# Optimization experiments

Hardware: AMD Instinct MI355X
Metric: run time of the kernel (lower is better)

## Reference

```python
import jax, jax.numpy as jnp
import numpy as np

B, C, TX, TY = 32, 384, 512, 2048
NL, K = 2, 3
EPS = 1e-5


def _ln(x, g, b):
    # channel-wise LayerNorm over dim 1 of [B, C, T]
    m = jnp.mean(x, axis=1, keepdims=True)
    v = jnp.mean((x - m) ** 2, axis=1, keepdims=True)
    return (x - m) * jax.lax.rsqrt(v + EPS) * g[None, :, None] + b[None, :, None]


def _conv(x, w, b):
    # x: [B, C, T], w: [O, I, K] -> 'SAME' padding == kernel_size // 2 for odd K
    y = jax.lax.conv_general_dilated(x, w, (1,), 'SAME',
                                     dimension_numbers=('NCH', 'OIH', 'NCH'))
    return y + b[None, :, None]


def _variance_predictor(x, mask, lng, lnb, cw, cb, ow, ob):
    # NL x (LayerNorm -> Conv1d -> SiLU -> [dropout=identity in eval]) * mask
    for i in range(NL):
        h = _conv(_ln(x, lng[i], lnb[i]), cw[i], cb[i])
        x = jax.nn.silu(h) * mask
    return _conv(x, ow, ob) * mask  # [B, 1, T]


def setup_inputs() -> dict:
    key = jax.random.key(0)
    it = iter(jax.random.split(key, 16))
    s = 0.02
    d = {}
    d['x'] = jax.random.normal(next(it), (B, C, TX), jnp.float32)
    d['x_mask'] = jnp.ones((B, 1, TX), jnp.float32)
    d['y_mask'] = jnp.ones((B, 1, TY), jnp.float32)
    d['pitch'] = jax.random.normal(next(it), (B, C, TY), jnp.float32)
    d['energy'] = jax.random.normal(next(it), (B, C, TY), jnp.float32)
    d['path'] = jax.random.uniform(next(it), (B, TX, TY), jnp.float32)
    for p in ('dur', 'pit', 'ene'):
        d[p + '_lng'] = jnp.ones((NL, C), jnp.float32)
        d[p + '_lnb'] = jnp.zeros((NL, C), jnp.float32)
        d[p + '_cw'] = jax.random.normal(next(it), (NL, C, C, K), jnp.float32) * s
        d[p + '_cb'] = jnp.zeros((NL, C), jnp.float32)
        d[p + '_ow'] = jax.random.normal(next(it), (1, C, 1), jnp.float32) * s
        d[p + '_ob'] = jnp.zeros((1,), jnp.float32)
    return d


def reference(x, x_mask, y_mask, pitch, energy, path,
              dur_lng, dur_lnb, dur_cw, dur_cb, dur_ow, dur_ob,
              pit_lng, pit_lnb, pit_cw, pit_cb, pit_ow, pit_ob,
              ene_lng, ene_lnb, ene_cw, ene_cb, ene_ow, ene_ob):
    dur_pred = _variance_predictor(x, x_mask, dur_lng, dur_lnb, dur_cw, dur_cb, dur_ow, dur_ob)
    # LengthRegulator: bmm against duration path matrix [B, TX, TY]
    xe = jnp.einsum('bct,bty->bcy', x, path)  # [B, C, TY]
    pitch_pred = _variance_predictor(xe, y_mask, pit_lng, pit_lnb, pit_cw, pit_cb, pit_ow, pit_ob)
    energy_pred = _variance_predictor(xe, y_mask, ene_lng, ene_lnb, ene_cw, ene_cb, ene_ow, ene_ob)
    out = xe + pitch + energy
    return (out, dur_pred, pitch_pred, energy_pred)
```

## Files before the change

kernel.cpp:

```cpp
#include <hip/hip_runtime.h>

#define B_ 32
#define C_ 384
#define TX_ 512
#define TY_ 2048
#define EPS_ 1e-5f
#define LAY_ ((size_t)(36 * 1536 * 8))

typedef __attribute__((ext_vector_type(8))) short short8;
typedef __attribute__((ext_vector_type(4))) float f32x4;

#define MFMA(a, b, c) __builtin_amdgcn_mfma_f32_16x16x32_bf16(a, b, c, 0, 0, 0)

#define WAITV(N) do { asm volatile("s_waitcnt vmcnt(" #N ")"); \
                      __builtin_amdgcn_sched_barrier(0); } while (0)
#define WAITLK(N) do { asm volatile("s_waitcnt lgkmcnt(" #N ")"); \
                       __builtin_amdgcn_sched_barrier(0); } while (0)
#define SB() __builtin_amdgcn_sched_barrier(0)

typedef unsigned int u32;
__device__ __forceinline__ void gl_lds16(const void* g, void* l) {
    __builtin_amdgcn_global_load_lds(
        (const __attribute__((address_space(1))) u32*)g,
        (__attribute__((address_space(3))) u32*)l, 16, 0, 0);
}

__device__ inline unsigned short f2bf(float f) {
    union { float f; unsigned int u; } v; v.f = f;
    unsigned int r = v.u + 0x7fffu + ((v.u >> 16) & 1u);
    return (unsigned short)(r >> 16);
}
__device__ inline float bf2f(unsigned short s) {
    union { float f; unsigned int u; } v; v.u = ((unsigned int)s) << 16;
    return v.f;
}

template<bool INBF>
__device__ inline float ldx(const void* p, size_t i) {
    if constexpr (INBF) return bf2f(((const unsigned short*)p)[i]);
    else return ((const float*)p)[i];
}

__global__ __launch_bounds__(256) void pack_w2(const float* cw0, const float* cw1,
                                               const float* cw2, const float* g0,
                                               const float* g1, const float* g2,
                                               unsigned short* wp) {
    int idx = blockIdx.x * 256 + threadIdx.x;
    const int NG = 6 * 36 * 384 * 4;
    if (idx >= NG) return;
    int lg = idx & 3;
    int o = (idx >> 2) % 384;
    int c = ((idx >> 2) / 384) % 36;
    int lay = (idx >> 2) / (384 * 36);
    int k = c / 12, ib = c % 12;
    int pr = lay >> 1, l = lay & 1;
    const float* cw = ((pr == 0) ? cw0 : (pr == 1) ? cw1 : cw2) + (size_t)l * C_ * C_ * 3;
    const float* g  = ((pr == 0) ? g0  : (pr == 1) ? g1  : g2)  + (size_t)l * C_;
    const int i0 = ib * 32 + lg * 8;
    short8 v;
    #pragma unroll
    for (int e = 0; e < 8; e++)
        v[e] = (short)f2bf(cw[((size_t)o * C_ + i0 + e) * 3 + k] * g[i0 + e]);
    *(short8*)&wp[(size_t)idx * 8] = v;
}

__global__ __launch_bounds__(256) void bias_fold(
    const float* cw0, const float* cw1, const float* cw2,
    const float* be0, const float* be1, const float* be2,
    const float* cb0, const float* cb1, const float* cb2,
    float* biasT, float* bc0, float* bc2) {
    int idx = blockIdx.x * 256 + threadIdx.x;
    if (idx >= 6 * 384) return;
    int o = idx % 384, lay = idx / 384;
    int pr = lay >> 1, l = lay & 1;
    const float* cw = ((pr == 0) ? cw0 : (pr == 1) ? cw1 : cw2)
                      + (size_t)l * C_ * C_ * 3 + (size_t)o * C_ * 3;
    const float* be = ((pr == 0) ? be0 : (pr == 1) ? be1 : be2) + (size_t)l * C_;
    const float* cb = ((pr == 0) ? cb0 : (pr == 1) ? cb1 : cb2) + (size_t)l * C_;
    float s0 = 0.f, s1 = 0.f, s2 = 0.f;
    for (int i = 0; i < C_; i++) {
        const float b = be[i];
        s0 += cw[i * 3 + 0] * b; s1 += cw[i * 3 + 1] * b; s2 += cw[i * 3 + 2] * b;
    }
    biasT[idx] = cb[o] + s0 + s1 + s2;
    bc0[idx] = s0; bc2[idx] = s2;
}

__global__ __launch_bounds__(256) void pack_x2(const float* x, unsigned short* xp) {
    int idx = blockIdx.x * 256 + threadIdx.x;
    const int NG = B_ * 16 * 384 * 4;
    if (idx >= NG) return;
    int lg = idx & 3;
    int c = (idx >> 2) % 384;
    int q = ((idx >> 2) / 384) % 16;
    int b = (idx >> 2) / (384 * 16);
    const float* src = x + ((size_t)b * C_ + c) * TX_ + q * 32 + lg * 8;
    short8 v;
    #pragma unroll
    for (int e = 0; e < 8; e++) v[e] = (short)f2bf(src[e]);
    *(short8*)&xp[(size_t)idx * 8] = v;
}

__global__ __launch_bounds__(256) void ln_stats_f32(const float* x, float2* st, int T) {
    __shared__ float r1[4][64], r2[4][64];
    int b = blockIdx.y, t0 = blockIdx.x * 64;
    int tl = threadIdx.x & 63, g = threadIdx.x >> 6;
    int t = t0 + tl;
    const float* p = x + (size_t)b * C_ * T + t;
    float s = 0.f, ss = 0.f;
    for (int c = g; c < C_; c += 4) { float v = p[(size_t)c * T]; s += v; ss += v * v; }
    r1[g][tl] = s; r2[g][tl] = ss;
    __syncthreads();
    if (threadIdx.x < 64) {
        float s1 = r1[0][tl] + r1[1][tl] + r1[2][tl] + r1[3][tl];
        float s2 = r2[0][tl] + r2[1][tl] + r2[2][tl] + r2[3][tl];
        float m = s1 * (1.f / C_);
        float var = s2 * (1.f / C_) - m * m;
        st[(size_t)b * T + t0 + tl] = make_float2(m, rsqrtf(var + EPS_));
    }
}

template<bool INBF>
__global__ __launch_bounds__(512, 2) void fused_vp(
    const void* __restrict__ Xin, const float2* __restrict__ stin,
    const unsigned short* __restrict__ W2lay,
    const float* __restrict__ bT,
    const float* __restrict__ c0v, const float* __restrict__ c2v,
    const float* __restrict__ mask,
    float* __restrict__ pred, const float* __restrict__ ow,
    const float* __restrict__ obias, int T)
{
    __shared__ __align__(16) unsigned short xs[132 * 384];
    __shared__ __align__(16) unsigned short wlds[8][2][1536];
    __shared__ float red[260];
    __shared__ float2 st2[130];

    const int tid = threadIdx.x;
    const int b = blockIdx.y;
    const int t0 = blockIdx.x * 128;
    const int lane = tid & 63;
    const int wave = tid >> 6;
    const int lr = lane & 15, lg = lane >> 4;
    const int wm = wave * 48;

    const unsigned short* gbw = W2lay + (size_t)((wm + lr) * 4 + lg) * 8;
    const unsigned short* gbw2 = gbw + LAY_;
    auto STAGE = [&](const unsigned short* base, int c, int buf) {
        #pragma unroll
        for (int fm = 0; fm < 3; fm++)
            gl_lds16(base + (size_t)c * 12288 + fm * 512, &wlds[wave][buf][fm * 512]);
    };
    STAGE(gbw, 0, 0);
    STAGE(gbw, 1, 1);

    {
        const int tl = tid & 127;
        const int tt = 2 + tl;
        const int t = t0 + tl;
        const float2 mr = stin[(size_t)b * T + t];
        const int cg0 = (tid >> 7) * 12;
        for (int i = 0; i < 12; i++) {
            const int cg = cg0 + i;
            const size_t base = ((size_t)b * C_ + cg * 8) * T + t;
            short8 v8;
            #pragma unroll
            for (int j = 0; j < 8; j++)
                v8[j] = (short)f2bf((ldx<INBF>(Xin, base + (size_t)j * T) - mr.x) * mr.y);
            const int ph = (cg & ~7) | ((cg ^ tt) & 7);
            *(short8*)&xs[tt * 384 + ph * 8] = v8;
        }
        if (tid < 192) {
            const int q = tid / 48;
            const int tt2 = (q < 2) ? q : 128 + q;
            const int cg = tid % 48;
            const int t2 = t0 - 2 + tt2;
            short8 v8;
            if (t2 >= 0 && t2 < T) {
                const float2 mr2 = stin[(size_t)b * T + t2];
                const size_t base = ((size_t)b * C_ + cg * 8) * T + t2;
                #pragma unroll
                for (int j = 0; j < 8; j++)
                    v8[j] = (short)f2bf((ldx<INBF>(Xin, base + (size_t)j * T) - mr2.x) * mr2.y);
            } else {
                #pragma unroll
                for (int j = 0; j < 8; j++) v8[j] = 0;
            }
            const int ph = (cg & ~7) | ((cg ^ tt2) & 7);
            *(short8*)&xs[tt2 * 384 + ph * 8] = v8;
        }
    }
    __syncthreads();

    f32x4 acc[3][9];
    const f32x4 zero = {0.f, 0.f, 0.f, 0.f};
    #pragma unroll
    for (int fm = 0; fm < 3; fm++)
        #pragma unroll
        for (int fn = 0; fn < 9; fn++) acc[fm][fn] = zero;

    short8 af[3], bfA[9], bfB[9];
    auto LOADBF1 = [&](short8* dst, int c) {
        const int k = c / 12, ib = c - k * 12;
        const int cgi = ib * 4 + lg;
        #pragma unroll
        for (int fn = 0; fn < 8; fn++) {
            const int row = 1 + fn * 16 + lr + k;
            const int ph = (cgi & ~7) | ((cgi ^ row) & 7);
            dst[fn] = *(const short8*)&xs[row * 384 + ph * 8];
        }
        const int rowh = (lr == 1) ? (129 + k) : k;
        const int phh = (cgi & ~7) | ((cgi ^ rowh) & 7);
        dst[8] = *(const short8*)&xs[rowh * 384 + phh * 8];
    };
    auto LOADAF = [&](int c) {
        #pragma unroll
        for (int fm = 0; fm < 3; fm++)
            af[fm] = *(const short8*)&wlds[wave][c & 1][fm * 512 + lane * 8];
    };
    auto FMAS1 = [&](short8* bf) {
        __builtin_amdgcn_s_setprio(1);
        #pragma unroll
        for (int fm = 0; fm < 3; fm++)
            #pragma unroll
            for (int fn = 0; fn < 9; fn++)
                acc[fm][fn] = MFMA(af[fm], bf[fn], acc[fm][fn]);
        __builtin_amdgcn_s_setprio(0);
    };
    auto STAGE1 = [&](int s) {
        if (s + 2 < 36) STAGE(gbw, s + 2, s & 1);
        else            STAGE(gbw2, s - 34, s & 1);
    };

    LOADBF1(bfA, 0);
    for (int c = 0; c < 36; c += 2) {
        WAITV(3);
        LOADAF(c); SB();
        LOADBF1(bfB, c + 1);
        WAITLK(9);
        STAGE1(c); SB();
        FMAS1(bfA);
        WAITV(3);
        LOADAF(c + 1); SB();
        LOADBF1(bfA, (c + 2 < 36) ? c + 2 : 35);
        WAITLK(9);
        STAGE1(c + 1); SB();
        FMAS1(bfB);
    }

    __syncthreads();
    if (tid < 260) red[tid] = 0.f;
    __syncthreads();

    #pragma unroll
    for (int fn = 0; fn < 8; fn++) {
        const int tt_h = 1 + fn * 16 + lr;
        const int t = t0 + fn * 16 + lr;
        const float mk = mask[(size_t)b * T + t];
        float s1 = 0.f, s2 = 0.f;
        #pragma unroll
        for (int fm = 0; fm < 3; fm++) {
            const int o0 = wm + fm * 16 + lg * 4;
            #pragma unroll
            for (int j = 0; j < 4; j++) {
                float h = acc[fm][fn][j] + bT[o0 + j];
                if (t == 0) h -= c0v[o0 + j];
                if (t == T - 1) h -= c2v[o0 + j];
                const float y = h * (1.f / (1.f + __expf(-h))) * mk;
                acc[fm][fn][j] = y;
                s1 += y; s2 += y * y;
            }
        }
        atomicAdd(&red[tt_h * 2], s1);
        atomicAdd(&red[tt_h * 2 + 1], s2);
    }
    {
        const int tt_h = (lr == 1) ? 129 : 0;
        const int t = t0 - 1 + tt_h;
        const bool inr = (lr < 2) && (t >= 0) && (t < T);
        const float mk = inr ? mask[(size_t)b * T + t] : 0.f;
        float s1 = 0.f, s2 = 0.f;
        #pragma unroll
        for (int fm = 0; fm < 3; fm++) {
            const int o0 = wm + fm * 16 + lg * 4;
            #pragma unroll
            for (int j = 0; j < 4; j++) {
                const float h = acc[fm][8][j] + bT[o0 + j];
                const float y = inr ? (h * (1.f / (1.f + __expf(-h))) * mk) : 0.f;
                acc[fm][8][j] = y;
                s1 += y; s2 += y * y;
            }
        }
        if (inr) {
            atomicAdd(&red[tt_h * 2], s1);
            atomicAdd(&red[tt_h * 2 + 1], s2);
        }
    }
    __syncthreads();

    if (tid < 130) {
        const float s1 = red[tid * 2], s2 = red[tid * 2 + 1];
        const float m = s1 * (1.f / C_);
        const float var = s2 * (1.f / C_) - m * m;
        st2[tid] = make_float2(m, rsqrtf(var + EPS_));
    }
    __syncthreads();

    #pragma unroll
    for (int fn = 0; fn < 8; fn++) {
        const int tt_h = 1 + fn * 16 + lr;
        const float2 mr = st2[tt_h];
        #pragma unroll
        for (int fm = 0; fm < 3; fm++) {
            ushort4 pk;
            #pragma unroll
            for (int j = 0; j < 4; j++)
                ((unsigned short*)&pk)[j] = f2bf((acc[fm][fn][j] - mr.x) * mr.y);
            const int cg = ((wm + fm * 16) >> 3) + (lg >> 1);
            const int ph = (cg & ~7) | ((cg ^ tt_h) & 7);
            *(ushort4*)&xs[tt_h * 384 + ph * 8 + (lg & 1) * 4] = pk;
        }
    }
    if (lr < 2) {
        const int tt_h = (lr == 1) ? 129 : 0;
        const float2 mr = st2[tt_h];
        #pragma unroll
        for (int fm = 0; fm < 3; fm++) {
            ushort4 pk;
            #pragma unroll
            for (int j = 0; j < 4; j++)
                ((unsigned short*)&pk)[j] = f2bf((acc[fm][8][j] - mr.x) * mr.y);
            const int cg = ((wm + fm * 16) >> 3) + (lg >> 1);
            const int ph = (cg & ~7) | ((cg ^ tt_h) & 7);
            *(ushort4*)&xs[tt_h * 384 + ph * 8 + (lg & 1) * 4] = pk;
        }
    }
    __syncthreads();

    f32x4 acc2[3][8];
    #pragma unroll
    for (int fm = 0; fm < 3; fm++)
        #pragma unroll
        for (int fn = 0; fn < 8; fn++) acc2[fm][fn] = zero;

    auto LOADBF2 = [&](short8* dst, int c) {
        const int k = c / 12, ib = c - k * 12;
        const int cgi = ib * 4 + lg;
        #pragma unroll
        for (int fn = 0; fn < 8; fn++) {
            const int row = fn * 16 + lr + k;
            const int ph = (cgi & ~7) | ((cgi ^ row) & 7);
            dst[fn] = *(const short8*)&xs[row * 384 + ph * 8];
        }
    };
    auto FMAS2 = [&](short8* bf) {
        __builtin_amdgcn_s_setprio(1);
        #pragma unroll
        for (int fm = 0; fm < 3; fm++)
            #pragma unroll
            for (int fn = 0; fn < 8; fn++)
                acc2[fm][fn] = MFMA(af[fm], bf[fn], acc2[fm][fn]);
        __builtin_amdgcn_s_setprio(0);
    };
    auto STAGE2 = [&](int s) {
        STAGE(gbw2, (s + 2 < 36) ? s + 2 : 35, s & 1);
    };

    LOADBF2(bfA, 0);
    for (int c = 0; c < 36; c += 2) {
        WAITV(3);
        LOADAF(c); SB();
        LOADBF2(bfB, c + 1);
        WAITLK(8);
        STAGE2(c); SB();
        FMAS2(bfA);
        WAITV(3);
        LOADAF(c + 1); SB();
        LOADBF2(bfA, (c + 2 < 36) ? c + 2 : 35);
        WAITLK(8);
        STAGE2(c + 1); SB();
        FMAS2(bfB);
    }

    __syncthreads();
    if (tid < 128) red[tid] = 0.f;
    __syncthreads();
    #pragma unroll
    for (int fn = 0; fn < 8; fn++) {
        const int tl = fn * 16 + lr;
        const int t = t0 + tl;
        const float mk = mask[(size_t)b * T + t];
        float s1 = 0.f;
        #pragma unroll
        for (int fm = 0; fm < 3; fm++) {
            const int o0 = wm + fm * 16 + lg * 4;
            #pragma unroll
            for (int j = 0; j < 4; j++) {
                float h = acc2[fm][fn][j] + bT[384 + o0 + j];
                if (t == 0) h -= c0v[384 + o0 + j];
                if (t == T - 1) h -= c2v[384 + o0 + j];
                const float y = h * (1.f / (1.f + __expf(-h))) * mk;
                s1 += y * ow[o0 + j];
            }
        }
        atomicAdd(&red[tl], s1);
    }
    __syncthreads();
    if (tid < 128) {
        const int t = t0 + tid;
        pred[(size_t)b * T + t] = (red[tid] + obias[0]) * mask[(size_t)b * T + t];
    }
}

__global__ __launch_bounds__(512, 2) void bmm_ln(
    const unsigned short* __restrict__ x2, const float* __restrict__ path,
    const float* __restrict__ pitch, const float* __restrict__ energy,
    float* __restrict__ out, unsigned short* __restrict__ xebf,
    float2* __restrict__ stout, int fused)
{
    __shared__ __align__(16) char smem[81920];
    unsigned short* ps = (unsigned short*)smem;
    typedef unsigned short wbuf_t[2][1536];
    wbuf_t* wlds = (wbuf_t*)(smem + 32768);
    float* red = (float*)(smem + 49152);

    const int tid = threadIdx.x;
    const int bid = blockIdx.x;
    const int work = (bid & 7) * 64 + (bid >> 3);
    const int b = work >> 4;
    const int y0 = (work & 15) << 7;
    const int lane = tid & 63;
    const int wave = tid >> 6;
    const int lr = lane & 15, lg = lane >> 4;
    const int wm = wave * 48;

    const unsigned short* gbx = x2 + ((size_t)b * 16 * 1536 + (size_t)((wm + lr) * 4 + lg)) * 8;
    auto STAGEW = [&](int u, int buf) {
        #pragma unroll
        for (int fm = 0; fm < 3; fm++)
            gl_lds16(gbx + (size_t)u * 12288 + fm * 512, &wlds[wave][buf][fm * 512]);
    };
    STAGEW(0, 0);
    STAGEW(1, 1);

    auto STAGEP = [&](int s) {
        const int yy = tid & 127;
        const int tg = tid >> 7;
        const float* pb = path + ((size_t)b * TX_ + s * 128 + tg * 32) * TY_ + y0 + yy;
        #pragma unroll
        for (int g = 0; g < 4; g++) {
            float vv[8];
            #pragma unroll
            for (int j = 0; j < 8; j++) vv[j] = pb[(size_t)(g * 8 + j) * TY_];
            short8 v8;
            #pragma unroll
            for (int j = 0; j < 8; j++) v8[j] = (short)f2bf(vv[j]);
            const int cg = tg * 4 + g;
            const int ph = (cg & ~7) | ((cg ^ yy) & 7);
            *(short8*)&ps[yy * 128 + ph * 8] = v8;
        }
    };

    f32x4 acc[3][8];
    const f32x4 zero = {0.f, 0.f, 0.f, 0.f};
    #pragma unroll
    for (int fm = 0; fm < 3; fm++)
        #pragma unroll
        for (int fn = 0; fn < 8; fn++) acc[fm][fn] = zero;

    short8 af[3], bfA[8], bfB[8];
    auto LOADAF = [&](int u) {
        #pragma unroll
        for (int fm = 0; fm < 3; fm++)
            af[fm] = *(const short8*)&wlds[wave][u & 1][fm * 512 + lane * 8];
    };
    auto LOADBF = [&](short8* dst, int uu) {
        const int cgi = uu * 4 + lg;
        #pragma unroll
        for (int fn = 0; fn < 8; fn++) {
            const int row = fn * 16 + lr;
            const int ph = (cgi & ~7) | ((cgi ^ row) & 7);
            dst[fn] = *(const short8*)&ps[row * 128 + ph * 8];
        }
    };
    auto FMAS = [&](short8* bf) {
        __builtin_amdgcn_s_setprio(1);
        #pragma unroll
        for (int fm = 0; fm < 3; fm++)
            #pragma unroll
            for (int fn = 0; fn < 8; fn++)
                acc[fm][fn] = MFMA(af[fm], bf[fn], acc[fm][fn]);
        __builtin_amdgcn_s_setprio(0);
    };

    for (int s = 0; s < 4; ++s) {
        if (s) __syncthreads();
        STAGEP(s);
        __syncthreads();
        const int u0 = s * 4;
        LOADBF(bfA, 0);
        WAITV(3); LOADAF(u0); SB();
        LOADBF(bfB, 1);
        WAITLK(8); STAGEW((u0 + 2 < 16) ? u0 + 2 : 15, u0 & 1); SB();
        FMAS(bfA);
        WAITV(3); LOADAF(u0 + 1); SB();
        LOADBF(bfA, 2);
        WAITLK(8); STAGEW((u0 + 3 < 16) ? u0 + 3 : 15, (u0 + 1) & 1); SB();
        FMAS(bfB);
        WAITV(3); LOADAF(u0 + 2); SB();
        LOADBF(bfB, 3);
        WAITLK(8); STAGEW((u0 + 4 < 16) ? u0 + 4 : 15, (u0 + 2) & 1); SB();
        FMAS(bfA);
        WAITV(3); LOADAF(u0 + 3); SB();
        WAITLK(0); STAGEW((u0 + 5 < 16) ? u0 + 5 : 15, (u0 + 3) & 1); SB();
        FMAS(bfB);
    }
    WAITV(0);

    __syncthreads();
    if (tid < 256) red[tid] = 0.f;
    __syncthreads();
    #pragma unroll
    for (int fn = 0; fn < 8; fn++) {
        const int yl = fn * 16 + lr;
        float s1 = 0.f, s2 = 0.f;
        #pragma unroll
        for (int fm = 0; fm < 3; fm++)
            #pragma unroll
            for (int j = 0; j < 4; j++) {
                const float v = acc[fm][fn][j];
                s1 += v; s2 += v * v;
            }
        atomicAdd(&red[yl * 2], s1);
        atomicAdd(&red[yl * 2 + 1], s2);
    }

    float* psf = (float*)smem;
    for (int r = 0; r < 4; ++r) {
        __syncthreads();
        if ((wave >> 1) == r) {
            const int cbase = (wave & 1) * 48;
            #pragma unroll
            for (int fn = 0; fn < 8; fn++) {
                const int yl = fn * 16 + lr;
                #pragma unroll
                for (int fm = 0; fm < 3; fm++) {
                    const int cl = cbase + fm * 16 + lg * 4;
                    #pragma unroll
                    for (int j = 0; j < 4; j++)
                        psf[(cl + j) * 128 + yl] = acc[fm][fn][j];
                }
            }
        }
        __syncthreads();
        for (int idx = tid; idx < 96 * 32; idx += 512) {
            const int cl = idx >> 5;
            const int y4 = idx & 31;
            const int c = 96 * r + cl;
            const size_t gi = ((size_t)b * C_ + c) * TY_ + y0 + y4 * 4;
            float4 v = ((float4*)&psf[cl * 128])[y4];
            if (fused) {
                const float4 p = *(const float4*)&pitch[gi];
                const float4 e = *(const float4*)&energy[gi];
                float4 o;
                o.x = v.x + p.x + e.x; o.y = v.y + p.y + e.y;
                o.z = v.z + p.z + e.z; o.w = v.w + p.w + e.w;
                *(float4*)&out[gi] = o;
                ushort4 xb;
                xb.x = f2bf(v.x); xb.y = f2bf(v.y); xb.z = f2bf(v.z); xb.w = f2bf(v.w);
                *(ushort4*)&xebf[gi] = xb;
            } else {
                *(float4*)&out[gi] = v;
            }
        }
    }
    __syncthreads();
    if (tid < 128) {
        const int y = y0 + tid;
        const float s1 = red[tid * 2], s2 = red[tid * 2 + 1];
        const float m = s1 * (1.f / C_);
        const float var = s2 * (1.f / C_) - m * m;
        stout[(size_t)b * TY_ + y] = make_float2(m, rsqrtf(var + EPS_));
    }
}

__global__ __launch_bounds__(256) void add3(float4* o, const float4* p, const float4* e, int n4) {
    for (int i = blockIdx.x * 256 + threadIdx.x; i < n4; i += gridDim.x * 256) {
        float4 a = o[i], x1 = p[i], x2 = e[i];
        a.x += x1.x + x2.x; a.y += x1.y + x2.y;
        a.z += x1.z + x2.z; a.w += x1.w + x2.w;
        o[i] = a;
    }
}

extern "C" void kernel_launch(void* const* d_in, const int* in_sizes, int n_in,
                              void* d_out, int out_size, void* d_ws, size_t ws_size,
                              hipStream_t stream)
{
    const float* x      = (const float*)d_in[0];
    const float* x_mask = (const float*)d_in[1];
    const float* y_mask = (const float*)d_in[2];
    const float* pitch  = (const float*)d_in[3];
    const float* energy = (const float*)d_in[4];
    const float* path   = (const float*)d_in[5];
    const float* prm[3][6];
    for (int p = 0; p < 3; p++)
        for (int q = 0; q < 6; q++)
            prm[p][q] = (const float*)d_in[6 + p * 6 + q];

    float* out         = (float*)d_out;
    float* dur_pred    = out + (size_t)B_ * C_ * TY_;
    float* pitch_pred  = dur_pred + B_ * TX_;
    float* energy_pred = pitch_pred + B_ * TY_;

    const size_t BCTY = (size_t)B_ * C_ * TY_;
    char* w = (char*)d_ws;
    auto alloc = [&](size_t bytes) { char* r = w; w += (bytes + 255) & ~(size_t)255; return r; };

    unsigned short* W2   = (unsigned short*)alloc(6 * LAY_ * 2);
    float* biasT         = (float*)alloc(6 * 384 * 4);
    float* bc0           = (float*)alloc(6 * 384 * 4);
    float* bc2           = (float*)alloc(6 * 384 * 4);
    float2* stA          = (float2*)alloc((size_t)B_ * TY_ * 8);
    unsigned short* x2p  = (unsigned short*)alloc((size_t)B_ * 196608 * 2);
    size_t base_end = (size_t)(w - (char*)d_ws);
    unsigned short* xebf = (unsigned short*)alloc(BCTY * 2);
    size_t xe_end = (size_t)(w - (char*)d_ws);

    const bool haveXe = (xe_end <= ws_size);
    if (base_end > ws_size) return;

    pack_w2<<<dim3((6 * 36 * 384 * 4 + 255) / 256), 256, 0, stream>>>(
        prm[0][2], prm[1][2], prm[2][2], prm[0][0], prm[1][0], prm[2][0], W2);
    bias_fold<<<dim3(9), 256, 0, stream>>>(
        prm[0][2], prm[1][2], prm[2][2], prm[0][1], prm[1][1], prm[2][1],
        prm[0][3], prm[1][3], prm[2][3], biasT, bc0, bc2);
    pack_x2<<<dim3((B_ * 16 * 384 * 4 + 255) / 256), 256, 0, stream>>>(x, x2p);
    ln_stats_f32<<<dim3(TX_ / 64, B_), 256, 0, stream>>>(x, stA, TX_);

    fused_vp<false><<<dim3(TX_ / 128, B_), 512, 0, stream>>>(
        x, stA, W2, biasT, bc0, bc2, x_mask,
        dur_pred, prm[0][4], prm[0][5], TX_);

    bmm_ln<<<dim3(512, 1, 1), 512, 0, stream>>>(
        x2p, path, pitch, energy, out, haveXe ? xebf : nullptr, stA, haveXe ? 1 : 0);

    if (haveXe) {
        fused_vp<true><<<dim3(TY_ / 128, B_), 512, 0, stream>>>(
            xebf, stA, W2 + 2 * LAY_, biasT + 2 * 384, bc0 + 2 * 384, bc2 + 2 * 384,
            y_mask, pitch_pred, prm[1][4], prm[1][5], TY_);
        fused_vp<true><<<dim3(TY_ / 128, B_), 512, 0, stream>>>(
            xebf, stA, W2 + 4 * LAY_, biasT + 4 * 384, bc0 + 4 * 384, bc2 + 4 * 384,
            y_mask, energy_pred, prm[2][4], prm[2][5], TY_);
    } else {
        fused_vp<false><<<dim3(TY_ / 128, B_), 512, 0, stream>>>(
            out, stA, W2 + 2 * LAY_, biasT + 2 * 384, bc0 + 2 * 384, bc2 + 2 * 384,
            y_mask, pitch_pred, prm[1][4], prm[1][5], TY_);
        fused_vp<false><<<dim3(TY_ / 128, B_), 512, 0, stream>>>(
            out, stA, W2 + 4 * LAY_, biasT + 4 * 384, bc0 + 4 * 384, bc2 + 4 * 384,
            y_mask, energy_pred, prm[2][4], prm[2][5], TY_);
        add3<<<dim3(2048), 256, 0, stream>>>((float4*)out, (const float4*)pitch,
                                             (const float4*)energy, B_ * C_ * TY_ / 4);
    }
}
```

Baseline: 577.3 us.

## Halve fused_vp time tile and load weights directly from global to raise occupancy

The fused variance-predictor kernel now processes 64 time steps per block instead of 128, which shrinks the LDS activation tile and the accumulator arrays. Launch bounds go from 2 to 4 blocks per CU. The LDS-staged weight pipeline (global_load_lds with explicit waitcnt scheduling) is replaced by direct register loads of weight fragments, double-buffered in registers. The goal is more resident waves to hide latency, at the cost of twice as many blocks, more weight traffic per output element, and more halo-row overhead.

```diff
diff --git a/kernel.cpp b/kernel.cpp
--- a/kernel.cpp
+++ b/kernel.cpp
@@ -121,7 +121,7 @@
 }
 
 template<bool INBF>
-__global__ __launch_bounds__(512, 2) void fused_vp(
+__global__ __launch_bounds__(512, 4) void fused_vp(
     const void* __restrict__ Xin, const float2* __restrict__ stin,
     const unsigned short* __restrict__ W2lay,
     const float* __restrict__ bT,
@@ -130,14 +130,13 @@
     float* __restrict__ pred, const float* __restrict__ ow,
     const float* __restrict__ obias, int T)
 {
-    __shared__ __align__(16) unsigned short xs[132 * 384];
-    __shared__ __align__(16) unsigned short wlds[8][2][1536];
-    __shared__ float red[260];
-    __shared__ float2 st2[130];
+    __shared__ __align__(16) unsigned short xs[68 * 384];
+    __shared__ float red[132];
+    __shared__ float2 st2[66];
 
     const int tid = threadIdx.x;
     const int b = blockIdx.y;
-    const int t0 = blockIdx.x * 128;
+    const int t0 = blockIdx.x * 64;
     const int lane = tid & 63;
     const int wave = tid >> 6;
     const int lr = lane & 15, lg = lane >> 4;
@@ -145,22 +144,13 @@
 
     const unsigned short* gbw = W2lay + (size_t)((wm + lr) * 4 + lg) * 8;
     const unsigned short* gbw2 = gbw + LAY_;
-    auto STAGE = [&](const unsigned short* base, int c, int buf) {
-        #pragma unroll
-        for (int fm = 0; fm < 3; fm++)
-            gl_lds16(base + (size_t)c * 12288 + fm * 512, &wlds[wave][buf][fm * 512]);
-    };
-    STAGE(gbw, 0, 0);
-    STAGE(gbw, 1, 1);
 
     {
-        const int tl = tid & 127;
-        const int tt = 2 + tl;
-        const int t = t0 + tl;
+        const int tt = 2 + lane;
+        const int t = t0 + lane;
         const float2 mr = stin[(size_t)b * T + t];
-        const int cg0 = (tid >> 7) * 12;
-        for (int i = 0; i < 12; i++) {
-            const int cg = cg0 + i;
+        for (int i = 0; i < 6; i++) {
+            const int cg = wave + 8 * i;
             const size_t base = ((size_t)b * C_ + cg * 8) * T + t;
             short8 v8;
             #pragma unroll
@@ -171,7 +161,7 @@
         }
         if (tid < 192) {
             const int q = tid / 48;
-            const int tt2 = (q < 2) ? q : 128 + q;
+            const int tt2 = (q < 2) ? q : 64 + q;
             const int cg = tid % 48;
             const int t2 = t0 - 2 + tt2;
             short8 v8;
@@ -191,68 +181,64 @@
     }
     __syncthreads();
 
-    f32x4 acc[3][9];
+    f32x4 acc[3][5];
     const f32x4 zero = {0.f, 0.f, 0.f, 0.f};
     #pragma unroll
     for (int fm = 0; fm < 3; fm++)
         #pragma unroll
-        for (int fn = 0; fn < 9; fn++) acc[fm][fn] = zero;
-
-    short8 af[3], bfA[9], bfB[9];
-    auto LOADBF1 = [&](short8* dst, int c) {
+        for (int fn = 0; fn < 5; fn++) acc[fm][fn] = zero;
+
+    short8 afA[3], afB[3], bf[5];
+    auto LOADW = [&](short8* d, const unsigned short* base, int c) {
+        #pragma unroll
+        for (int fm = 0; fm < 3; fm++)
+            d[fm] = *(const short8*)(base + (size_t)c * 12288 + fm * 512);
+    };
+    auto LOADBF1 = [&](int c) {
         const int k = c / 12, ib = c - k * 12;
         const int cgi = ib * 4 + lg;
         #pragma unroll
-        for (int fn = 0; fn < 8; fn++) {
+        for (int fn = 0; fn < 4; fn++) {
             const int row = 1 + fn * 16 + lr + k;
             const int ph = (cgi & ~7) | ((cgi ^ row) & 7);
-            dst[fn] = *(const short8*)&xs[row * 384 + ph * 8];
-        }
-        const int rowh = (lr == 1) ? (129 + k) : k;
+            bf[fn] = *(const short8*)&xs[row * 384 + ph * 8];
+        }
+        const int rowh = (lr == 1) ? (65 + k) : k;
         const int phh = (cgi & ~7) | ((cgi ^ rowh) & 7);
-        dst[8] = *(const short8*)&xs[rowh * 384 + phh * 8];
-    };
-    auto LOADAF = [&](int c) {
+        bf[4] = *(const short8*)&xs[rowh * 384 + phh * 8];
+    };
+    auto FMAS1 = [&](short8* af) {
+        __builtin_amdgcn_s_setprio(1);
         #pragma unroll
         for (int fm = 0; fm < 3; fm++)
-            af[fm] = *(const short8*)&wlds[wave][c & 1][fm * 512 + lane * 8];
-    };
-    auto FMAS1 = [&](short8* bf) {
-        __builtin_amdgcn_s_setprio(1);
-        #pragma unroll
-        for (int fm = 0; fm < 3; fm++)
-            #pragma unroll
-            for (int fn = 0; fn < 9; fn++)
+            #pragma unroll
+            for (int fn = 0; fn < 5; fn++)
                 acc[fm][fn] = MFMA(af[fm], bf[fn], acc[fm][fn]);
         __builtin_amdgcn_s_setprio(0);
     };
-    auto STAGE1 = [&](int s) {
-        if (s + 2 < 36) STAGE(gbw, s + 2, s & 1);
-        else            STAGE(gbw2, s - 34, s & 1);
-    };
-
-    LOADBF1(bfA, 0);
-    for (int c = 0; c < 36; c += 2) {
-        WAITV(3);
-        LOADAF(c); SB();
-        LOADBF1(bfB, c + 1);
-        WAITLK(9);
-        STAGE1(c); SB();
-        FMAS1(bfA);
-        WAITV(3);
-        LOADAF(c + 1); SB();
-        LOADBF1(bfA, (c + 2 < 36) ? c + 2 : 35);
-        WAITLK(9);
-        STAGE1(c + 1); SB();
-        FMAS1(bfB);
-    }
-
-    __syncthreads();
-    if (tid < 260) red[tid] = 0.f;
-    __syncthreads();
-
-    #pragma unroll
-    for (int fn = 0; fn < 8; fn++) {
+
+    LOADW(afA, gbw, 0);
+    #pragma unroll 2
+    for (int c = 0; c < 36; ++c) {
+        const unsigned short* nb = (c + 1 < 36) ? gbw : gbw2;
+        const int nc = (c + 1 < 36) ? c + 1 : 0;
+        if ((c & 1) == 0) {
+            LOADW(afB, nb, nc);
+            LOADBF1(c);
+            FMAS1(afA);
+        } else {
+            LOADW(afA, nb, nc);
+            LOADBF1(c);
+            FMAS1(afB);
+        }
+    }
+
+    __syncthreads();
+    if (tid < 132) red[tid] = 0.f;
+    __syncthreads();
+
+    #pragma unroll
+    for (int fn = 0; fn < 4; fn++) {
         const int tt_h = 1 + fn * 16 + lr;
         const int t = t0 + fn * 16 + lr;
         const float mk = mask[(size_t)b * T + t];
@@ -274,7 +260,7 @@
         atomicAdd(&red[tt_h * 2 + 1], s2);
     }
     {
-        const int tt_h = (lr == 1) ? 129 : 0;
+        const int tt_h = (lr == 1) ? 65 : 0;
         const int t = t0 - 1 + tt_h;
         const bool inr = (lr < 2) && (t >= 0) && (t < T);
         const float mk = inr ? mask[(size_t)b * T + t] : 0.f;
@@ -284,9 +270,9 @@
             const int o0 = wm + fm * 16 + lg * 4;
             #pragma unroll
             for (int j = 0; j < 4; j++) {
-                const float h = acc[fm][8][j] + bT[o0 + j];
+                const float h = acc[fm][4][j] + bT[o0 + j];
                 const float y = inr ? (h * (1.f / (1.f + __expf(-h))) * mk) : 0.f;
-                acc[fm][8][j] = y;
+                acc[fm][4][j] = y;
                 s1 += y; s2 += y * y;
             }
         }
@@ -297,7 +283,7 @@
     }
     __syncthreads();
 
-    if (tid < 130) {
+    if (tid < 66) {
         const float s1 = red[tid * 2], s2 = red[tid * 2 + 1];
         const float m = s1 * (1.f / C_);
         const float var = s2 * (1.f / C_) - m * m;
@@ -306,7 +292,7 @@
     __syncthreads();
 
     #pragma unroll
-    for (int fn = 0; fn < 8; fn++) {
+    for (int fn = 0; fn < 4; fn++) {
         const int tt_h = 1 + fn * 16 + lr;
         const float2 mr = st2[tt_h];
         #pragma unroll
@@ -321,14 +307,14 @@
         }
     }
     if (lr < 2) {
-        const int tt_h = (lr == 1) ? 129 : 0;
+        const int tt_h = (lr == 1) ? 65 : 0;
         const float2 mr = st2[tt_h];
         #pragma unroll
         for (int fm = 0; fm < 3; fm++) {
             ushort4 pk;
             #pragma unroll
             for (int j = 0; j < 4; j++)
-                ((unsigned short*)&pk)[j] = f2bf((acc[fm][8][j] - mr.x) * mr.y);
+                ((unsigned short*)&pk)[j] = f2bf((acc[fm][4][j] - mr.x) * mr.y);
             const int cg = ((wm + fm * 16) >> 3) + (lg >> 1);
             const int ph = (cg & ~7) | ((cg ^ tt_h) & 7);
             *(ushort4*)&xs[tt_h * 384 + ph * 8 + (lg & 1) * 4] = pk;
@@ -336,56 +322,51 @@
     }
     __syncthreads();
 
-    f32x4 acc2[3][8];
+    f32x4 acc2[3][4];
     #pragma unroll
     for (int fm = 0; fm < 3; fm++)
         #pragma unroll
-        for (int fn = 0; fn < 8; fn++) acc2[fm][fn] = zero;
-
-    auto LOADBF2 = [&](short8* dst, int c) {
+        for (int fn = 0; fn < 4; fn++) acc2[fm][fn] = zero;
+
+    auto LOADBF2 = [&](int c) {
         const int k = c / 12, ib = c - k * 12;
         const int cgi = ib * 4 + lg;
         #pragma unroll
-        for (int fn = 0; fn < 8; fn++) {
+        for (int fn = 0; fn < 4; fn++) {
             const int row = fn * 16 + lr + k;
             const int ph = (cgi & ~7) | ((cgi ^ row) & 7);
-            dst[fn] = *(const short8*)&xs[row * 384 + ph * 8];
-        }
-    };
-    auto FMAS2 = [&](short8* bf) {
+            bf[fn] = *(const short8*)&xs[row * 384 + ph * 8];
+        }
+    };
+    auto FMAS2 = [&](short8* af) {
         __builtin_amdgcn_s_setprio(1);
         #pragma unroll
         for (int fm = 0; fm < 3; fm++)
             #pragma unroll
-            for (int fn = 0; fn < 8; fn++)
+            for (int fn = 0; fn < 4; fn++)
                 acc2[fm][fn] = MFMA(af[fm], bf[fn], acc2[fm][fn]);
         __builtin_amdgcn_s_setprio(0);
     };
-    auto STAGE2 = [&](int s) {
-        STAGE(gbw2, (s + 2 < 36) ? s + 2 : 35, s & 1);
-    };
-
-    LOADBF2(bfA, 0);
-    for (int c = 0; c < 36; c += 2) {
-        WAITV(3);
-        LOADAF(c); SB();
-        LOADBF2(bfB, c + 1);
-        WAITLK(8);
-        STAGE2(c); SB();
-        FMAS2(bfA);
-        WAITV(3);
-        LOADAF(c + 1); SB();
-        LOADBF2(bfA, (c + 2 < 36) ? c + 2 : 35);
-        WAITLK(8);
-        STAGE2(c + 1); SB();
-        FMAS2(bfB);
-    }
-
-    __syncthreads();
-    if (tid < 128) red[tid] = 0.f;
-    __syncthreads();
-    #pragma unroll
-    for (int fn = 0; fn < 8; fn++) {
+
+    #pragma unroll 2
+    for (int c = 0; c < 36; ++c) {
+        const int nc = (c + 1 < 36) ? c + 1 : 35;
+        if ((c & 1) == 0) {
+            LOADW(afB, gbw2, nc);
+            LOADBF2(c);
+            FMAS2(afA);
+        } else {
+            LOADW(afA, gbw2, nc);
+            LOADBF2(c);
+            FMAS2(afB);
+        }
+    }
+
+    __syncthreads();
+    if (tid < 64) red[tid] = 0.f;
+    __syncthreads();
+    #pragma unroll
+    for (int fn = 0; fn < 4; fn++) {
         const int tl = fn * 16 + lr;
         const int t = t0 + tl;
         const float mk = mask[(size_t)b * T + t];
@@ -405,7 +386,7 @@
         atomicAdd(&red[tl], s1);
     }
     __syncthreads();
-    if (tid < 128) {
+    if (tid < 64) {
         const int t = t0 + tid;
         pred[(size_t)b * T + t] = (red[tid] + obias[0]) * mask[(size_t)b * T + t];
     }
@@ -637,7 +618,7 @@
     pack_x2<<<dim3((B_ * 16 * 384 * 4 + 255) / 256), 256, 0, stream>>>(x, x2p);
     ln_stats_f32<<<dim3(TX_ / 64, B_), 256, 0, stream>>>(x, stA, TX_);
 
-    fused_vp<false><<<dim3(TX_ / 128, B_), 512, 0, stream>>>(
+    fused_vp<false><<<dim3(TX_ / 64, B_), 512, 0, stream>>>(
         x, stA, W2, biasT, bc0, bc2, x_mask,
         dur_pred, prm[0][4], prm[0][5], TX_);
 
@@ -645,17 +626,17 @@
         x2p, path, pitch, energy, out, haveXe ? xebf : nullptr, stA, haveXe ? 1 : 0);
 
     if (haveXe) {
-        fused_vp<true><<<dim3(TY_ / 128, B_), 512, 0, stream>>>(
+        fused_vp<true><<<dim3(TY_ / 64, B_), 512, 0, stream>>>(
             xebf, stA, W2 + 2 * LAY_, biasT + 2 * 384, bc0 + 2 * 384, bc2 + 2 * 384,
             y_mask, pitch_pred, prm[1][4], prm[1][5], TY_);
-        fused_vp<true><<<dim3(TY_ / 128, B_), 512, 0, stream>>>(
+        fused_vp<true><<<dim3(TY_ / 64, B_), 512, 0, stream>>>(
             xebf, stA, W2 + 4 * LAY_, biasT + 4 * 384, bc0 + 4 * 384, bc2 + 4 * 384,
             y_mask, energy_pred, prm[2][4], prm[2][5], TY_);
     } else {
-        fused_vp<false><<<dim3(TY_ / 128, B_), 512, 0, stream>>>(
+        fused_vp<false><<<dim3(TY_ / 64, B_), 512, 0, stream>>>(
             out, stA, W2 + 2 * LAY_, biasT + 2 * 384, bc0 + 2 * 384, bc2 + 2 * 384,
             y_mask, pitch_pred, prm[1][4], prm[1][5], TY_);
-        fused_vp<false><<<dim3(TY_ / 128, B_), 512, 0, stream>>>(
+        fused_vp<false><<<dim3(TY_ / 64, B_), 512, 0, stream>>>(
             out, stA, W2 + 4 * LAY_, biasT + 4 * 384, bc0 + 4 * 384, bc2 + 4 * 384,
             y_mask, energy_pred, prm[2][4], prm[2][5], TY_);
         add3<<<dim3(2048), 256, 0, stream>>>((float4*)out, (const float4*)pitch,
```

Result: no change. 579.6 us (+0.4%).
